# Kernel tuning notes

Hardware: AMD Instinct MI355X
Metric: run time of the kernel (lower is better)

The kernel has to match this reference:

```python
import jax, jax.numpy as jnp
import numpy as np

N = 16384        # number of nodes
F_IN = 128       # dim_nodes
H = 128          # hidden_channels
OUT = 2


def setup_inputs() -> dict:
    key = jax.random.key(0)
    ks = jax.random.split(key, 8)
    x = jax.random.normal(ks[0], (N, F_IN), dtype=jnp.float32)
    adjacency = jax.random.uniform(ks[1], (N, N), dtype=jnp.float32)
    # GCNConv weights (aggregate then linear) and final head
    w1 = jax.random.normal(ks[2], (F_IN, H), dtype=jnp.float32) / np.sqrt(F_IN)
    b1 = jnp.zeros((H,), dtype=jnp.float32)
    w2 = jax.random.normal(ks[3], (H, H), dtype=jnp.float32) / np.sqrt(H)
    b2 = jnp.zeros((H,), dtype=jnp.float32)
    w3 = jax.random.normal(ks[4], (H, OUT), dtype=jnp.float32) / np.sqrt(H)
    b3 = jnp.zeros((OUT,), dtype=jnp.float32)
    return {"x": x, "adjacency": adjacency, "w1": w1, "b1": b1,
            "w2": w2, "b2": b2, "w3": w3, "b3": b3}


def reference(x, adjacency, w1, b1, w2, b2, w3, b3):
    # GCNConv layer 1: adjacency aggregation + linear, then ReLU
    h = jax.nn.relu(adjacency @ (x @ w1) + b1)      # [N, H]
    # GCNConv layer 2
    h = jax.nn.relu(adjacency @ (h @ w2) + b2)      # [N, H]
    # dropout p=0.5 is identity at inference (training=False)
    # Linear head -> 2 classes
    return h @ w3 + b3                              # [N, 2]
```

## Files before the change

### kernel.cpp

```cpp
#include <hip/hip_runtime.h>

typedef __bf16 bf16_t;
typedef __bf16 bf16x8 __attribute__((ext_vector_type(8)));
typedef float f32x4 __attribute__((ext_vector_type(4)));

constexpr int NN = 16384;
constexpr int F  = 128;
constexpr int BM = 64;
constexpr int BK = 64;
constexpr int LDA = 72;
constexpr int LDB = 72;

template<bool IN_BF16>
__global__ __launch_bounds__(256)
void small_gemm_T(const void* __restrict__ inp, const float* __restrict__ w,
                  bf16_t* __restrict__ outT)
{
    __shared__ float xt[32 * 132];
    const int t  = threadIdx.x;
    const int i0 = blockIdx.x * 32;
    {
        const int r = t >> 3, cc = (t & 7) * 16;
        float* dst = &xt[r * 132 + cc];
        if constexpr (!IN_BF16) {
            const float* src = (const float*)inp + (size_t)(i0 + r) * F + cc;
            float4 v0 = ((const float4*)src)[0];
            float4 v1 = ((const float4*)src)[1];
            float4 v2 = ((const float4*)src)[2];
            float4 v3 = ((const float4*)src)[3];
            ((float4*)dst)[0] = v0; ((float4*)dst)[1] = v1;
            ((float4*)dst)[2] = v2; ((float4*)dst)[3] = v3;
        } else {
            const bf16_t* src = (const bf16_t*)inp + (size_t)(i0 + r) * F + cc;
            bf16x8 v0 = ((const bf16x8*)src)[0];
            bf16x8 v1 = ((const bf16x8*)src)[1];
            #pragma unroll
            for (int q = 0; q < 8; q++) { dst[q] = (float)v0[q]; dst[8 + q] = (float)v1[q]; }
        }
    }
    __syncthreads();
    const int j  = t & 127;
    const int r0 = (t >> 7) * 16;
    float acc[16];
    #pragma unroll
    for (int r = 0; r < 16; r++) acc[r] = 0.f;
    for (int k4 = 0; k4 < F / 4; k4++) {
        const float w0 = w[(k4 * 4 + 0) * F + j];
        const float w1v = w[(k4 * 4 + 1) * F + j];
        const float w2v = w[(k4 * 4 + 2) * F + j];
        const float w3v = w[(k4 * 4 + 3) * F + j];
        #pragma unroll
        for (int r = 0; r < 16; r++) {
            const float4 xv = *(const float4*)&xt[(r0 + r) * 132 + k4 * 4];
            acc[r] += xv.x * w0 + xv.y * w1v + xv.z * w2v + xv.w * w3v;
        }
    }
    bf16_t* dst = outT + (size_t)j * NN + i0 + r0;
    #pragma unroll
    for (int r = 0; r < 16; r++) dst[r] = (bf16_t)acc[r];
}

template<bool FINAL>
__global__ __launch_bounds__(256)
void agg_gemm(const float* __restrict__ Aadj, const bf16_t* __restrict__ BT,
              const float* __restrict__ bias, bf16_t* __restrict__ Hout,
              const float* __restrict__ w3, const float* __restrict__ b3,
              float* __restrict__ out)
{
    __shared__ bf16_t sA[BM * LDA];
    __shared__ bf16_t sB[F * LDB];
    const int t = threadIdx.x;
    const int m0 = blockIdx.x * BM;
    const int w = t >> 6, lane = t & 63, quad = lane >> 4, l16 = lane & 15;

    f32x4 acc[4][2];
    #pragma unroll
    for (int mf = 0; mf < 4; mf++)
        #pragma unroll
        for (int nf = 0; nf < 2; nf++) acc[mf][nf] = (f32x4){0.f, 0.f, 0.f, 0.f};

    const int am = t >> 2, ac = (t & 3) * 16;
    const float* aptr = Aadj + (size_t)(m0 + am) * NN + ac;
    bf16_t* sA_dst = &sA[am * LDA + ac];
    const int bn = t >> 1, bc = (t & 1) * 32;
    const bf16_t* bptr = BT + (size_t)bn * NN + bc;
    bf16_t* sB_dst = &sB[bn * LDB + bc];

    float4 av[4];
    bf16x8 bv[4];
    {
        const float4* ap = (const float4*)aptr;
        av[0] = ap[0]; av[1] = ap[1]; av[2] = ap[2]; av[3] = ap[3];
        const bf16x8* bp = (const bf16x8*)bptr;
        bv[0] = bp[0]; bv[1] = bp[1]; bv[2] = bp[2]; bv[3] = bp[3];
    }

    for (int k0 = 0; k0 < NN; k0 += BK) {
        {
            bf16x8 p0, p1;
            const float* fs = (const float*)av;
            #pragma unroll
            for (int q = 0; q < 8; q++) { p0[q] = (bf16_t)fs[q]; p1[q] = (bf16_t)fs[8 + q]; }
            ((bf16x8*)sA_dst)[0] = p0; ((bf16x8*)sA_dst)[1] = p1;
            ((bf16x8*)sB_dst)[0] = bv[0]; ((bf16x8*)sB_dst)[1] = bv[1];
            ((bf16x8*)sB_dst)[2] = bv[2]; ((bf16x8*)sB_dst)[3] = bv[3];
        }
        __syncthreads();
        {
            const int kn = (k0 + BK < NN) ? (k0 + BK) : 0;
            const float4* ap = (const float4*)(aptr + kn);
            av[0] = ap[0]; av[1] = ap[1]; av[2] = ap[2]; av[3] = ap[3];
            const bf16x8* bp = (const bf16x8*)(bptr + kn);
            bv[0] = bp[0]; bv[1] = bp[1]; bv[2] = bp[2]; bv[3] = bp[3];
        }
        #pragma unroll
        for (int ks = 0; ks < 2; ks++) {
            bf16x8 afr[4], bfr[2];
            #pragma unroll
            for (int mf = 0; mf < 4; mf++)
                afr[mf] = *(const bf16x8*)&sA[(mf * 16 + l16) * LDA + ks * 32 + quad * 8];
            #pragma unroll
            for (int nf = 0; nf < 2; nf++)
                bfr[nf] = *(const bf16x8*)&sB[(w * 32 + nf * 16 + l16) * LDB + ks * 32 + quad * 8];
            #pragma unroll
            for (int mf = 0; mf < 4; mf++)
                #pragma unroll
                for (int nf = 0; nf < 2; nf++)
                    acc[mf][nf] = __builtin_amdgcn_mfma_f32_16x16x32_bf16(
                        afr[mf], bfr[nf], acc[mf][nf], 0, 0, 0);
        }
        __syncthreads();
    }

    if constexpr (!FINAL) {
        #pragma unroll
        for (int mf = 0; mf < 4; mf++)
            #pragma unroll
            for (int nf = 0; nf < 2; nf++) {
                const int col = w * 32 + nf * 16 + l16;
                const float bvs = bias[col];
                #pragma unroll
                for (int r = 0; r < 4; r++) {
                    const int row = m0 + mf * 16 + quad * 4 + r;
                    float v = acc[mf][nf][r] + bvs;
                    v = v > 0.f ? v : 0.f;
                    Hout[(size_t)row * F + col] = (bf16_t)v;
                }
            }
    } else {
        __shared__ float htile[BM * 132];
        #pragma unroll
        for (int mf = 0; mf < 4; mf++)
            #pragma unroll
            for (int nf = 0; nf < 2; nf++) {
                const int col = w * 32 + nf * 16 + l16;
                const float bvs = bias[col];
                #pragma unroll
                for (int r = 0; r < 4; r++) {
                    const int rl = mf * 16 + quad * 4 + r;
                    float v = acc[mf][nf][r] + bvs;
                    v = v > 0.f ? v : 0.f;
                    htile[rl * 132 + col] = v;
                }
            }
        __syncthreads();
        if (t < 128) {
            const int r = t >> 1, c = t & 1;
            float s = b3[c];
            for (int k = 0; k < F; k++) s += htile[r * 132 + k] * w3[k * 2 + c];
            out[(size_t)(m0 + r) * 2 + c] = s;
        }
    }
}

extern "C" void kernel_launch(void* const* d_in, const int* in_sizes, int n_in,
                              void* d_out, int out_size, void* d_ws, size_t ws_size,
                              hipStream_t stream)
{
    const float* x   = (const float*)d_in[0];
    const float* adj = (const float*)d_in[1];
    const float* w1  = (const float*)d_in[2];
    const float* b1  = (const float*)d_in[3];
    const float* w2  = (const float*)d_in[4];
    const float* b2  = (const float*)d_in[5];
    const float* w3  = (const float*)d_in[6];
    const float* b3  = (const float*)d_in[7];
    float* out = (float*)d_out;

    bf16_t* xw1T = (bf16_t*)d_ws;
    bf16_t* h1   = xw1T + (size_t)F * NN;
    bf16_t* hw2T = h1   + (size_t)NN * F;

    small_gemm_T<false><<<NN / 32, 256, 0, stream>>>((const void*)x, w1, xw1T);
    agg_gemm<false><<<NN / BM, 256, 0, stream>>>(adj, xw1T, b1, h1, nullptr, nullptr, nullptr);
    small_gemm_T<true><<<NN / 32, 256, 0, stream>>>((const void*)h1, w2, hw2T);
    agg_gemm<true><<<NN / BM, 256, 0, stream>>>(adj, hw2T, b2, nullptr, w3, b3, out);
}
```

Baseline: 1.848 ms.

## Split-K the adjacency aggregation GEMMs and reduce partials in finish kernels

```diff
diff --git a/kernel.cpp b/kernel.cpp
--- a/kernel.cpp
+++ b/kernel.cpp
@@ -2,6 +2,7 @@
 
 typedef __bf16 bf16_t;
 typedef __bf16 bf16x8 __attribute__((ext_vector_type(8)));
+typedef __bf16 bf16x4 __attribute__((ext_vector_type(4)));
 typedef float f32x4 __attribute__((ext_vector_type(4)));
 
 constexpr int NN = 16384;
@@ -10,6 +11,8 @@
 constexpr int BK = 64;
 constexpr int LDA = 72;
 constexpr int LDB = 72;
+constexpr int SPLITK = 4;
+constexpr int KSPAN  = NN / SPLITK;
 
 template<bool IN_BF16>
 __global__ __launch_bounds__(256)
@@ -60,17 +63,17 @@
     for (int r = 0; r < 16; r++) dst[r] = (bf16_t)acc[r];
 }
 
-template<bool FINAL>
-__global__ __launch_bounds__(256)
-void agg_gemm(const float* __restrict__ Aadj, const bf16_t* __restrict__ BT,
-              const float* __restrict__ bias, bf16_t* __restrict__ Hout,
-              const float* __restrict__ w3, const float* __restrict__ b3,
-              float* __restrict__ out)
+__global__ __launch_bounds__(256, 4)
+void agg_gemm_split(const float* __restrict__ Aadj, const bf16_t* __restrict__ BT,
+                    float* __restrict__ Ppart)
 {
     __shared__ bf16_t sA[BM * LDA];
     __shared__ bf16_t sB[F * LDB];
     const int t = threadIdx.x;
     const int m0 = blockIdx.x * BM;
+    const int kq = blockIdx.y;
+    const int kbeg = kq * KSPAN;
+    const int kend = kbeg + KSPAN;
     const int w = t >> 6, lane = t & 63, quad = lane >> 4, l16 = lane & 15;
 
     f32x4 acc[4][2];
@@ -86,16 +89,19 @@
     const bf16_t* bptr = BT + (size_t)bn * NN + bc;
     bf16_t* sB_dst = &sB[bn * LDB + bc];
 
-    float4 av[4];
+    f32x4 av[4];
     bf16x8 bv[4];
     {
-        const float4* ap = (const float4*)aptr;
-        av[0] = ap[0]; av[1] = ap[1]; av[2] = ap[2]; av[3] = ap[3];
-        const bf16x8* bp = (const bf16x8*)bptr;
+        const f32x4* ap = (const f32x4*)(aptr + kbeg);
+        av[0] = __builtin_nontemporal_load(ap + 0);
+        av[1] = __builtin_nontemporal_load(ap + 1);
+        av[2] = __builtin_nontemporal_load(ap + 2);
+        av[3] = __builtin_nontemporal_load(ap + 3);
+        const bf16x8* bp = (const bf16x8*)(bptr + kbeg);
         bv[0] = bp[0]; bv[1] = bp[1]; bv[2] = bp[2]; bv[3] = bp[3];
     }
 
-    for (int k0 = 0; k0 < NN; k0 += BK) {
+    for (int k0 = kbeg; k0 < kend; k0 += BK) {
         {
             bf16x8 p0, p1;
             const float* fs = (const float*)av;
@@ -107,9 +113,12 @@
         }
         __syncthreads();
         {
-            const int kn = (k0 + BK < NN) ? (k0 + BK) : 0;
-            const float4* ap = (const float4*)(aptr + kn);
-            av[0] = ap[0]; av[1] = ap[1]; av[2] = ap[2]; av[3] = ap[3];
+            const int kn = (k0 + BK < kend) ? (k0 + BK) : kbeg;
+            const f32x4* ap = (const f32x4*)(aptr + kn);
+            av[0] = __builtin_nontemporal_load(ap + 0);
+            av[1] = __builtin_nontemporal_load(ap + 1);
+            av[2] = __builtin_nontemporal_load(ap + 2);
+            av[3] = __builtin_nontemporal_load(ap + 3);
             const bf16x8* bp = (const bf16x8*)(bptr + kn);
             bv[0] = bp[0]; bv[1] = bp[1]; bv[2] = bp[2]; bv[3] = bp[3];
         }
@@ -132,43 +141,75 @@
         __syncthreads();
     }
 
-    if constexpr (!FINAL) {
-        #pragma unroll
-        for (int mf = 0; mf < 4; mf++)
-            #pragma unroll
-            for (int nf = 0; nf < 2; nf++) {
-                const int col = w * 32 + nf * 16 + l16;
-                const float bvs = bias[col];
-                #pragma unroll
-                for (int r = 0; r < 4; r++) {
-                    const int row = m0 + mf * 16 + quad * 4 + r;
-                    float v = acc[mf][nf][r] + bvs;
-                    v = v > 0.f ? v : 0.f;
-                    Hout[(size_t)row * F + col] = (bf16_t)v;
-                }
+    float* dst = Ppart + (size_t)kq * NN * F;
+    #pragma unroll
+    for (int mf = 0; mf < 4; mf++)
+        #pragma unroll
+        for (int nf = 0; nf < 2; nf++) {
+            const int col = w * 32 + nf * 16 + l16;
+            #pragma unroll
+            for (int r = 0; r < 4; r++) {
+                const int row = m0 + mf * 16 + quad * 4 + r;
+                dst[(size_t)row * F + col] = acc[mf][nf][r];
             }
-    } else {
-        __shared__ float htile[BM * 132];
-        #pragma unroll
-        for (int mf = 0; mf < 4; mf++)
-            #pragma unroll
-            for (int nf = 0; nf < 2; nf++) {
-                const int col = w * 32 + nf * 16 + l16;
-                const float bvs = bias[col];
-                #pragma unroll
-                for (int r = 0; r < 4; r++) {
-                    const int rl = mf * 16 + quad * 4 + r;
-                    float v = acc[mf][nf][r] + bvs;
-                    v = v > 0.f ? v : 0.f;
-                    htile[rl * 132 + col] = v;
-                }
-            }
-        __syncthreads();
-        if (t < 128) {
-            const int r = t >> 1, c = t & 1;
-            float s = b3[c];
-            for (int k = 0; k < F; k++) s += htile[r * 132 + k] * w3[k * 2 + c];
-            out[(size_t)(m0 + r) * 2 + c] = s;
+        }
+}
+
+__global__ __launch_bounds__(256)
+void finish_h(const float* __restrict__ P, const float* __restrict__ bias,
+              bf16_t* __restrict__ h)
+{
+    const int g = blockIdx.x * 256 + threadIdx.x;
+    const int row = g >> 5;
+    const int c4  = g & 31;
+    const size_t off = (size_t)row * F + c4 * 4;
+    f32x4 s = *(const f32x4*)(P + off);
+    #pragma unroll
+    for (int kq = 1; kq < SPLITK; kq++)
+        s += *(const f32x4*)(P + (size_t)kq * NN * F + off);
+    const f32x4 b = *(const f32x4*)(bias + c4 * 4);
+    bf16x4 o;
+    #pragma unroll
+    for (int q = 0; q < 4; q++) {
+        float v = s[q] + b[q];
+        o[q] = (bf16_t)(v > 0.f ? v : 0.f);
+    }
+    *(bf16x4*)(h + off) = o;
+}
+
+__global__ __launch_bounds__(256)
+void finish_final(const float* __restrict__ P, const float* __restrict__ b2,
+                  const float* __restrict__ w3, const float* __restrict__ b3,
+                  float* __restrict__ out)
+{
+    const int t = threadIdx.x, w = t >> 6, l = t & 63;
+    const int base = blockIdx.x * 64;
+    const float w00 = w3[l * 2],        w01 = w3[l * 2 + 1];
+    const float w10 = w3[(l + 64) * 2], w11 = w3[(l + 64) * 2 + 1];
+    const float bb0 = b2[l], bb1 = b2[l + 64];
+    const float o0 = b3[0], o1 = b3[1];
+    for (int rr = 0; rr < 16; rr++) {
+        const int row = base + rr * 4 + w;
+        const float* p = P + (size_t)row * F;
+        float v0 = p[l], v1 = p[l + 64];
+        #pragma unroll
+        for (int kq = 1; kq < SPLITK; kq++) {
+            const float* pk = p + (size_t)kq * NN * F;
+            v0 += pk[l]; v1 += pk[l + 64];
+        }
+        v0 += bb0; v1 += bb1;
+        v0 = v0 > 0.f ? v0 : 0.f;
+        v1 = v1 > 0.f ? v1 : 0.f;
+        float p0 = v0 * w00 + v1 * w10;
+        float p1 = v0 * w01 + v1 * w11;
+        #pragma unroll
+        for (int off = 32; off > 0; off >>= 1) {
+            p0 += __shfl_down(p0, off);
+            p1 += __shfl_down(p1, off);
+        }
+        if (l == 0) {
+            out[(size_t)row * 2 + 0] = p0 + o0;
+            out[(size_t)row * 2 + 1] = p1 + o1;
         }
     }
 }
@@ -187,12 +228,17 @@
     const float* b3  = (const float*)d_in[7];
     float* out = (float*)d_out;
 
-    bf16_t* xw1T = (bf16_t*)d_ws;
-    bf16_t* h1   = xw1T + (size_t)F * NN;
-    bf16_t* hw2T = h1   + (size_t)NN * F;
+    bf16_t* xw1T  = (bf16_t*)d_ws;
+    bf16_t* h1    = xw1T + (size_t)F * NN;
+    bf16_t* hw2T  = h1   + (size_t)NN * F;
+    float*  Ppart = (float*)(hw2T + (size_t)F * NN);
+
+    dim3 agrid(NN / BM, SPLITK);
 
     small_gemm_T<false><<<NN / 32, 256, 0, stream>>>((const void*)x, w1, xw1T);
-    agg_gemm<false><<<NN / BM, 256, 0, stream>>>(adj, xw1T, b1, h1, nullptr, nullptr, nullptr);
+    agg_gemm_split<<<agrid, 256, 0, stream>>>(adj, xw1T, Ppart);
+    finish_h<<<NN * F / 4 / 256, 256, 0, stream>>>(Ppart, b1, h1);
     small_gemm_T<true><<<NN / 32, 256, 0, stream>>>((const void*)h1, w2, hw2T);
-    agg_gemm<true><<<NN / BM, 256, 0, stream>>>(adj, hw2T, b2, nullptr, w3, b3, out);
-}
+    agg_gemm_split<<<agrid, 256, 0, stream>>>(adj, hw2T, Ppart);
+    finish_final<<<NN / 64, 256, 0, stream>>>(Ppart, b2, w3, b3, out);
+}
```

Result: slower. 1.960 ms (+6.1%).
